# Optimization experiments

Hardware: AMD Instinct MI355X
Metric: run time of the kernel (lower is better)

Reference implementation:

```python
import jax, jax.numpy as jnp
import numpy as np
import math

EPS = 1e-07
LOG2PI = math.log(2.0 * math.pi)
ITERS = 3
FINAL_LAMBDA = 0.01


def setup_inputs() -> dict:
    key = jax.random.key(0)
    k1, k2, k3, k4 = jax.random.split(key, 4)
    B, oH, oW, KH, KW, IC, OC, P = 4, 12, 12, 3, 3, 16, 32, 16
    V = jax.random.normal(k1, (B, oH, oW, KH, KW, IC, OC, P), dtype=jnp.float32)
    a = jax.random.uniform(k2, (B, oH, oW, KH, KW, IC), dtype=jnp.float32)
    Beta_u = jax.random.normal(k3, (OC, 1), dtype=jnp.float32)
    Beta_a = jax.random.normal(k4, (OC,), dtype=jnp.float32)
    return {"V": V, "a": a, "Beta_u": Beta_u, "Beta_a": Beta_a,
            "outSize": (B, oH, oW, OC, P), "outCaps": OC}


def reference(V, a, Beta_u, Beta_a, outSize, outCaps):
    # R: [B,oH,oW,KH,KW,inCaps,outCaps]
    R = jnp.full(a.shape + (outCaps,), 1.0 / outCaps, dtype=V.dtype)
    a6 = a[..., None]  # [B,oH,oW,KH,KW,inCaps,1]
    for i in range(ITERS):
        Lambda = FINAL_LAMBDA * (1.0 - 0.95 ** (i + 1))
        Rw = (R * a6)[..., None]  # [...,inCaps,outCaps,1]
        mu_denom = Rw.sum(axis=(3, 4, 5), keepdims=True)  # [B,oH,oW,1,1,1,OC,1]
        mu = (Rw * V).sum(axis=(3, 4, 5), keepdims=True) / (mu_denom + EPS)
        V_mu_sqr = (V - mu) ** 2
        sigma_sqr = (Rw * V_mu_sqr).sum(axis=(3, 4, 5), keepdims=True) / (mu_denom + EPS)
        cost_h = (Beta_u + 0.5 * jnp.log(sigma_sqr)) * mu_denom
        x = Lambda * (Beta_a - cost_h.sum(axis=7))  # [B,oH,oW,1,1,1,OC]
        # F.normalize(x, dim=6): L2-normalize with eps=1e-12 clamp
        norm = jnp.maximum(jnp.sqrt((x * x).sum(axis=6, keepdims=True)), 1e-12)
        a_out = jax.nn.sigmoid(x / norm)
        log_p1 = -0.5 * (LOG2PI + jnp.log(sigma_sqr)).sum(axis=7) + EPS
        log_p2 = -(V_mu_sqr / (2.0 * sigma_sqr + EPS)).sum(axis=7)
        R = jax.nn.softmax(jnp.log(a_out) + log_p1 + log_p2, axis=6)
    mu_out = jnp.squeeze(mu).reshape(outSize)
    sigma_out = jnp.squeeze(sigma_sqr).reshape(outSize)
    return mu_out, jnp.squeeze(a_out), sigma_out
```

## Files before the change

### kernel.cpp

```cpp
#include <hip/hip_runtime.h>

#define NPOS 576
#define KTOT 144
#define NOC 32
#define OCP 512
#define NCQ 128
#define RPT 36
#define EPSF 1e-7f
#define LOG2PIF 1.83787706640934548356f

__global__ __launch_bounds__(512)
__attribute__((amdgpu_waves_per_eu(2, 2)))
void em_routing(
    const float* __restrict__ Vf, const float* __restrict__ Af,
    const float* __restrict__ Bup, const float* __restrict__ Bap,
    float* __restrict__ out)
{
  const int pos = blockIdx.x;
  const int t   = (int)threadIdx.x;
  const int w   = t >> 6;
  const int l   = t & 63;
  const int c   = (w << 4) | (l & 15);
  const int rs  = l >> 4;
  const int oc  = c >> 2;

  __shared__ float sA[KTOT];
  __shared__ float sL[KTOT][NOC];
  __shared__ float sX[NOC];
  __shared__ float sBase[NOC];

  const float4* __restrict__ V4 =
      (const float4*)(Vf + (size_t)pos * (KTOT * OCP));

  if (t < KTOT) sA[t] = Af[pos * KTOT + t];
  const float Bu = Bup[oc];
  const float Ba = Bap[oc];
  __syncthreads();

  float4 vloc[RPT];
  float  s0 = 0.f;
  float4 s1 = {0.f,0.f,0.f,0.f}, s2 = {0.f,0.f,0.f,0.f};
  #pragma unroll
  for (int r = 0; r < RPT; ++r) {
    const int k = rs + 4 * r;
    vloc[r] = V4[k * NCQ + c];
    const float wk = sA[k] * (1.0f / 32.0f);
    const float4 v = vloc[r];
    s0 += wk;
    s1.x += wk * v.x; s1.y += wk * v.y; s1.z += wk * v.z; s1.w += wk * v.w;
    s2.x += wk * v.x * v.x; s2.y += wk * v.y * v.y;
    s2.z += wk * v.z * v.z; s2.w += wk * v.w * v.w;
  }

  float4 mu, sig;
  float aout = 0.5f;

  for (int it = 0; it < 3; ++it) {
    const float lam = (it == 0) ? 5e-4f : (it == 1) ? 9.75e-4f : 1.42625e-3f;

    #pragma unroll
    for (int m = 16; m <= 32; m <<= 1) {
      s0   += __shfl_xor(s0,   m);
      s1.x += __shfl_xor(s1.x, m); s1.y += __shfl_xor(s1.y, m);
      s1.z += __shfl_xor(s1.z, m); s1.w += __shfl_xor(s1.w, m);
      s2.x += __shfl_xor(s2.x, m); s2.y += __shfl_xor(s2.y, m);
      s2.z += __shfl_xor(s2.z, m); s2.w += __shfl_xor(s2.w, m);
    }

    const float inv = 1.0f / (s0 + EPSF);
    mu.x = s1.x * inv; mu.y = s1.y * inv; mu.z = s1.z * inv; mu.w = s1.w * inv;
    sig.x = fmaxf(s2.x * inv - mu.x * mu.x, 1e-30f);
    sig.y = fmaxf(s2.y * inv - mu.y * mu.y, 1e-30f);
    sig.z = fmaxf(s2.z * inv - mu.z * mu.z, 1e-30f);
    sig.w = fmaxf(s2.w * inv - mu.w * mu.w, 1e-30f);

    float Lown = logf(sig.x) + logf(sig.y) + logf(sig.z) + logf(sig.w);
    float L1 = Lown + __shfl_xor(Lown, 1);
    const float L = L1 + __shfl_xor(L1, 2);

    const float x = lam * (Ba - s0 * (16.0f * Bu + 0.5f * L));
    if (rs == 0 && (l & 3) == 0) sX[oc] = x;
    __syncthreads();
    float ss = 0.f;
    #pragma unroll
    for (int j = 0; j < NOC; ++j) ss += sX[j] * sX[j];
    const float nrm = fmaxf(sqrtf(ss), 1e-12f);
    aout = 1.0f / (1.0f + expf(-x / nrm));

    if (it == 2) break;

    float4 c0q;
    c0q.x = 1.0f / (2.0f * sig.x + EPSF);
    c0q.y = 1.0f / (2.0f * sig.y + EPSF);
    c0q.z = 1.0f / (2.0f * sig.z + EPSF);
    c0q.w = 1.0f / (2.0f * sig.w + EPSF);
    if (rs == 0 && (l & 3) == 0)
      sBase[oc] = logf(aout) + (-0.5f * (16.0f * LOG2PIF + L) + EPSF);
    __syncthreads();

    #pragma unroll
    for (int r = 0; r < RPT; ++r) {
      const float4 v = vloc[r];
      const float dx = v.x - mu.x, dy = v.y - mu.y,
                  dz = v.z - mu.z, dw = v.w - mu.w;
      float q = dx * dx * c0q.x + dy * dy * c0q.y
              + dz * dz * c0q.z + dw * dw * c0q.w;
      q += __shfl_xor(q, 1);
      q += __shfl_xor(q, 2);
      if ((l & 3) == 0) sL[rs + 4 * r][oc] = q;
    }
    __syncthreads();

    #pragma unroll
    for (int j = 0; j < 9; ++j) {
      const int idx = t + 512 * j;
      const int kl = idx >> 5, o = idx & 31;
      const float val = sBase[o] - sL[kl][o];
      float mx = val;
      #pragma unroll
      for (int m = 1; m < 32; m <<= 1) mx = fmaxf(mx, __shfl_xor(mx, m, 32));
      const float e = expf(val - mx);
      float sum = e;
      #pragma unroll
      for (int m = 1; m < 32; m <<= 1) sum += __shfl_xor(sum, m, 32);
      sL[kl][o] = e * (sA[kl] / sum);
    }
    __syncthreads();

    s0 = 0.f;
    s1.x = s1.y = s1.z = s1.w = 0.f;
    s2.x = s2.y = s2.z = s2.w = 0.f;
    #pragma unroll
    for (int r = 0; r < RPT; ++r) {
      const float wk = sL[rs + 4 * r][oc];
      const float4 v = vloc[r];
      s0 += wk;
      s1.x += wk * v.x; s1.y += wk * v.y; s1.z += wk * v.z; s1.w += wk * v.w;
      s2.x += wk * v.x * v.x; s2.y += wk * v.y * v.y;
      s2.z += wk * v.z * v.z; s2.w += wk * v.w * v.w;
    }
  }

  if (rs == 0) {
    float4* __restrict__ out4 = (float4*)out;
    out4[(size_t)pos * NCQ + c]          = mu;
    out4[78336u + (size_t)pos * NCQ + c] = sig;
    if ((l & 3) == 0) out[294912u + (size_t)pos * NOC + oc] = aout;
  }
}

extern "C" void kernel_launch(void* const* d_in, const int* in_sizes, int n_in,
                              void* d_out, int out_size, void* d_ws, size_t ws_size,
                              hipStream_t stream) {
  em_routing<<<NPOS, 512, 0, stream>>>((const float*)d_in[0], (const float*)d_in[1],
                                       (const float*)d_in[2], (const float*)d_in[3],
                                       (float*)d_out);
}
```

Baseline: 110.8 us.

## Spill part of V cache to LDS as bf16 to raise occupancy

Keeps 22 of 36 V rows per thread in registers and stores the remaining 14 rows in shared memory packed as bf16, then raises the waves-per-EU target from 2 to 4. The aim is to cut register pressure so more blocks fit per CU and global-load latency is hidden better across the 576 blocks. In exchange it adds LDS traffic and unpack work in each routing pass, and introduces bf16 rounding on part of V, which changes numerical accuracy. LDS use per block grows by about 57KB, which may itself limit how many blocks can be resident.

```diff
diff --git a/kernel.cpp b/kernel.cpp
--- a/kernel.cpp
+++ b/kernel.cpp
@@ -5,12 +5,32 @@
 #define NOC 32
 #define OCP 512
 #define NCQ 128
-#define RPT 36
+#define RREG 22
+#define RTOT 36
+#define NLDSROW 56
 #define EPSF 1e-7f
 #define LOG2PIF 1.83787706640934548356f
 
+__device__ __forceinline__ unsigned short f2bf(float f) {
+  unsigned int x = __builtin_bit_cast(unsigned int, f);
+  unsigned int r = x + 0x7fffu + ((x >> 16) & 1u);
+  return (unsigned short)(r >> 16);
+}
+__device__ __forceinline__ float bf2f(unsigned short u) {
+  unsigned int x = ((unsigned int)u) << 16;
+  return __builtin_bit_cast(float, x);
+}
+__device__ __forceinline__ float4 unpack_bf4(uint2 u) {
+  float4 v;
+  v.x = bf2f((unsigned short)(u.x & 0xffffu));
+  v.y = bf2f((unsigned short)(u.x >> 16));
+  v.z = bf2f((unsigned short)(u.y & 0xffffu));
+  v.w = bf2f((unsigned short)(u.y >> 16));
+  return v;
+}
+
 __global__ __launch_bounds__(512)
-__attribute__((amdgpu_waves_per_eu(2, 2)))
+__attribute__((amdgpu_waves_per_eu(4, 4)))
 void em_routing(
     const float* __restrict__ Vf, const float* __restrict__ Af,
     const float* __restrict__ Bup, const float* __restrict__ Bap,
@@ -26,6 +46,7 @@
 
   __shared__ float sA[KTOT];
   __shared__ float sL[KTOT][NOC];
+  __shared__ uint2 sV[NLDSROW][NCQ + 1];
   __shared__ float sX[NOC];
   __shared__ float sBase[NOC];
 
@@ -37,11 +58,11 @@
   const float Ba = Bap[oc];
   __syncthreads();
 
-  float4 vloc[RPT];
+  float4 vloc[RREG];
   float  s0 = 0.f;
   float4 s1 = {0.f,0.f,0.f,0.f}, s2 = {0.f,0.f,0.f,0.f};
   #pragma unroll
-  for (int r = 0; r < RPT; ++r) {
+  for (int r = 0; r < RREG; ++r) {
     const int k = rs + 4 * r;
     vloc[r] = V4[k * NCQ + c];
     const float wk = sA[k] * (1.0f / 32.0f);
@@ -51,6 +72,23 @@
     s2.x += wk * v.x * v.x; s2.y += wk * v.y * v.y;
     s2.z += wk * v.z * v.z; s2.w += wk * v.w * v.w;
   }
+  #pragma unroll
+  for (int r = RREG; r < RTOT; ++r) {
+    const int k = rs + 4 * r;
+    const float4 vr = V4[k * NCQ + c];
+    uint2 u;
+    u.x = (unsigned)f2bf(vr.x) | ((unsigned)f2bf(vr.y) << 16);
+    u.y = (unsigned)f2bf(vr.z) | ((unsigned)f2bf(vr.w) << 16);
+    sV[k - 88][c] = u;
+    const float4 v = unpack_bf4(u);
+    const float wk = sA[k] * (1.0f / 32.0f);
+    s0 += wk;
+    s1.x += wk * v.x; s1.y += wk * v.y; s1.z += wk * v.z; s1.w += wk * v.w;
+    s2.x += wk * v.x * v.x; s2.y += wk * v.y * v.y;
+    s2.z += wk * v.z * v.z; s2.w += wk * v.w * v.w;
+  }
+
+#define GETV(r) ((r) < RREG ? vloc[(r)] : unpack_bf4(sV[rs + 4 * (r) - 88][c]))
 
   float4 mu, sig;
   float aout = 0.5f;
@@ -99,8 +137,8 @@
     __syncthreads();
 
     #pragma unroll
-    for (int r = 0; r < RPT; ++r) {
-      const float4 v = vloc[r];
+    for (int r = 0; r < RTOT; ++r) {
+      const float4 v = GETV(r);
       const float dx = v.x - mu.x, dy = v.y - mu.y,
                   dz = v.z - mu.z, dw = v.w - mu.w;
       float q = dx * dx * c0q.x + dy * dy * c0q.y
@@ -131,9 +169,9 @@
     s1.x = s1.y = s1.z = s1.w = 0.f;
     s2.x = s2.y = s2.z = s2.w = 0.f;
     #pragma unroll
-    for (int r = 0; r < RPT; ++r) {
+    for (int r = 0; r < RTOT; ++r) {
       const float wk = sL[rs + 4 * r][oc];
-      const float4 v = vloc[r];
+      const float4 v = GETV(r);
       s0 += wk;
       s1.x += wk * v.x; s1.y += wk * v.y; s1.z += wk * v.z; s1.w += wk * v.w;
       s2.x += wk * v.x * v.x; s2.y += wk * v.y * v.y;
```

New measurement: 216.0 us. +94.9%, slower.
